# Kernel optimization log

Hardware: AMD Instinct MI355X
Metric: run time of the kernel (lower is better)

The kernel has to match this reference:

```python
import jax, jax.numpy as jnp
import numpy as np

D_MODEL = 1024
HEADS = 16
D_K = D_MODEL // HEADS
D_FF = 4096
EPS = 1e-6


def setup_inputs() -> dict:
    key = jax.random.key(0)
    ks = jax.random.split(key, 20)
    B, S, D = 8, 1024, D_MODEL
    sc = 1.0 / np.sqrt(D)
    scf = 1.0 / np.sqrt(D_FF)
    inp = {
        "x": jax.random.normal(ks[0], (B, S, D), jnp.float32),
        "mask": jnp.ones((B, 1, 1, S), jnp.int32),
        "wq": jax.random.normal(ks[1], (D, D), jnp.float32) * sc,
        "bq": jnp.zeros((D,), jnp.float32),
        "wk": jax.random.normal(ks[2], (D, D), jnp.float32) * sc,
        "bk": jnp.zeros((D,), jnp.float32),
        "wv": jax.random.normal(ks[3], (D, D), jnp.float32) * sc,
        "bv": jnp.zeros((D,), jnp.float32),
        "wo": jax.random.normal(ks[4], (D, D), jnp.float32) * sc,
        "bo": jnp.zeros((D,), jnp.float32),
        "w1": jax.random.normal(ks[5], (D_FF, D), jnp.float32) * sc,
        "b1": jnp.zeros((D_FF,), jnp.float32),
        "w2": jax.random.normal(ks[6], (D, D_FF), jnp.float32) * scf,
        "b2": jnp.zeros((D,), jnp.float32),
        "g1": jnp.ones((D,), jnp.float32),
        "be1": jnp.zeros((D,), jnp.float32),
        "g2": jnp.ones((D,), jnp.float32),
        "be2": jnp.zeros((D,), jnp.float32),
    }
    return inp


def _layernorm(x, gamma, beta):
    # Faithful to custom LayerNorm: unbiased std (ddof=1), divide by (std+eps)
    mean = jnp.mean(x, axis=-1, keepdims=True)
    std = jnp.std(x, axis=-1, ddof=1, keepdims=True)
    return gamma * (x - mean) / (std + EPS) + beta


def _mha(x, mask, wq, bq, wk, bk, wv, bv, wo, bo):
    B, S, D = x.shape
    q = x @ wq.T + bq
    k = x @ wk.T + bk
    v = x @ wv.T + bv
    # [B,S,D] -> [B,H,S,dk]
    q = q.reshape(B, S, HEADS, D_K).transpose(0, 2, 1, 3)
    k = k.reshape(B, S, HEADS, D_K).transpose(0, 2, 1, 3)
    v = v.reshape(B, S, HEADS, D_K).transpose(0, 2, 1, 3)
    scores = jnp.einsum("bhqd,bhkd->bhqk", q, k) / np.sqrt(D_K).astype(np.float32)
    scores = jnp.where(mask == 0, jnp.float32(-1e9), scores)
    attn = jax.nn.softmax(scores, axis=-1)
    out = jnp.einsum("bhqk,bhkd->bhqd", attn, v)
    out = out.transpose(0, 2, 1, 3).reshape(B, S, D)
    return out @ wo.T + bo


def reference(x, mask, wq, bq, wk, bk, wv, bv, wo, bo, w1, b1, w2, b2, g1, be1, g2, be2):
    # residual 1: x + MHA(LN(x))
    h = _layernorm(x, g1, be1)
    x = x + _mha(h, mask, wq, bq, wk, bk, wv, bv, wo, bo)
    # residual 2: x + FFN(LN(x))
    h = _layernorm(x, g2, be2)
    ff = jax.nn.relu(h @ w1.T + b1) @ w2.T + b2
    return x + ff
```

## Files before the change

### kernel.cpp

```cpp
#include <hip/hip_runtime.h>

typedef __attribute__((ext_vector_type(8))) short short8;
typedef __attribute__((ext_vector_type(4))) short short4_t;
typedef __attribute__((ext_vector_type(4))) float floatx4;
typedef __attribute__((ext_vector_type(16))) float floatx16;

#define NTOK 8192
#define S_ 1024
#define DM 1024

__device__ __forceinline__ unsigned short f2b(float f) {
    union { float f; unsigned u; } v; v.f = f;
    unsigned r = v.u + 0x7FFF + ((v.u >> 16) & 1);
    return (unsigned short)(r >> 16);
}

__device__ __forceinline__ float b2f(unsigned short u) {
    union { unsigned u; float f; } v; v.u = ((unsigned)u) << 16;
    return v.f;
}

__device__ __forceinline__ void gl_lds16(const void* g, void* l) {
    __builtin_amdgcn_global_load_lds((const __attribute__((address_space(1))) void*)g,
                                     (__attribute__((address_space(3))) void*)l, 16, 0, 0);
}

__global__ __launch_bounds__(256) void prep_kernel(const float* __restrict__ wq,
                                                   const float* __restrict__ wk,
                                                   const float* __restrict__ wv,
                                                   const float* __restrict__ wo,
                                                   const float* __restrict__ w1,
                                                   const float* __restrict__ w2,
                                                   const float* __restrict__ bq,
                                                   const float* __restrict__ bk,
                                                   const float* __restrict__ bv,
                                                   const int* __restrict__ mask,
                                                   const float* __restrict__ x,
                                                   const float* __restrict__ g1,
                                                   const float* __restrict__ be1,
                                                   unsigned short* __restrict__ wqkv_bf,
                                                   unsigned short* __restrict__ wo_bf,
                                                   unsigned short* __restrict__ w1_bf,
                                                   unsigned short* __restrict__ w2_bf,
                                                   float* __restrict__ bqkv,
                                                   float* __restrict__ mbias,
                                                   int* __restrict__ mflags,
                                                   unsigned short* __restrict__ h_bf) {
    const int bid = blockIdx.x;
    const int t = threadIdx.x;
    if (bid < 12288) {
        const int q = bid * 256 + t;
        const float* src;
        unsigned short* dst;
        int lq;
        if (q < 786432) {
            src = (q < 262144) ? wq : (q < 524288 ? wk : wv);
            lq = q & 262143;
            dst = wqkv_bf + (size_t)(q >> 18) * 1048576;
        } else if (q < 1048576) {
            src = wo; lq = q - 786432; dst = wo_bf;
        } else if (q < 2097152) {
            src = w1; lq = q - 1048576; dst = w1_bf;
        } else {
            src = w2; lq = q - 2097152; dst = w2_bf;
        }
        const float4 v = *reinterpret_cast<const float4*>(src + (size_t)lq * 4);
        short4_t o;
        o.x = (short)f2b(v.x); o.y = (short)f2b(v.y);
        o.z = (short)f2b(v.z); o.w = (short)f2b(v.w);
        *reinterpret_cast<short4_t*>(dst + (size_t)lq * 4) = o;
        return;
    }
    if (bid == 12288) {
#pragma unroll
        for (int it = 0; it < 3; ++it) {
            const int q = t + it * 256;
            const float* src = (q < 256) ? bq : (q < 512 ? bk : bv);
            const int lq = q & 255;
            *reinterpret_cast<float4*>(bqkv + q * 4) =
                *reinterpret_cast<const float4*>(src + lq * 4);
        }
        return;
    }
    if (bid == 12289) {
#pragma unroll
        for (int it = 0; it < 8; ++it) {
            const int q = t + it * 256;
            const int4 m = *reinterpret_cast<const int4*>(mask + q * 4);
            float4 o;
            o.x = (m.x == 0) ? -1e9f : 0.f;
            o.y = (m.y == 0) ? -1e9f : 0.f;
            o.z = (m.z == 0) ? -1e9f : 0.f;
            o.w = (m.w == 0) ? -1e9f : 0.f;
            *reinterpret_cast<float4*>(mbias + q * 4) = o;
        }
        if (t < 128) {
            int f = 0;
            const int* mp = mask + t * 64;
#pragma unroll
            for (int k = 0; k < 64; ++k) f |= (mp[k] == 0) ? 1 : 0;
            mflags[t] = f;
        }
        return;
    }
    const int row = bid - 12290;
    const float4 xv = *reinterpret_cast<const float4*>(x + (size_t)row * DM + t * 4);
    float s = xv.x + xv.y + xv.z + xv.w;
#pragma unroll
    for (int off = 32; off > 0; off >>= 1) s += __shfl_down(s, off);
    __shared__ float red[8];
    const int wid = t >> 6, lane = t & 63;
    if (lane == 0) red[wid] = s;
    __syncthreads();
    const float mean = (red[0] + red[1] + red[2] + red[3]) * (1.f / 1024.f);
    const float dx = xv.x - mean, dy = xv.y - mean, dz = xv.z - mean, dw = xv.w - mean;
    float ss = dx * dx + dy * dy + dz * dz + dw * dw;
#pragma unroll
    for (int off = 32; off > 0; off >>= 1) ss += __shfl_down(ss, off);
    if (lane == 0) red[4 + wid] = ss;
    __syncthreads();
    const float var = (red[4] + red[5] + red[6] + red[7]) * (1.f / 1023.f);
    const float inv = 1.f / (sqrtf(var) + 1e-6f);
    const float4 gv = *reinterpret_cast<const float4*>(g1 + t * 4);
    const float4 bev = *reinterpret_cast<const float4*>(be1 + t * 4);
    short4_t o;
    o.x = (short)f2b(gv.x * dx * inv + bev.x);
    o.y = (short)f2b(gv.y * dy * inv + bev.y);
    o.z = (short)f2b(gv.z * dz * inv + bev.z);
    o.w = (short)f2b(gv.w * dw * inv + bev.w);
    *reinterpret_cast<short4_t*>(h_bf + (size_t)row * DM + t * 4) = o;
}

__global__ __launch_bounds__(256) void ln_bf16(const unsigned short* __restrict__ xb,
                                               const float* __restrict__ g,
                                               const float* __restrict__ be,
                                               unsigned short* __restrict__ out) {
    const int row = blockIdx.x;
    const int t = threadIdx.x;
    const short4_t xv4 = *reinterpret_cast<const short4_t*>(xb + (size_t)row * DM + t * 4);
    float xv[4];
#pragma unroll
    for (int j = 0; j < 4; ++j) xv[j] = b2f((unsigned short)xv4[j]);
    float s = xv[0] + xv[1] + xv[2] + xv[3];
#pragma unroll
    for (int off = 32; off > 0; off >>= 1) s += __shfl_down(s, off);
    __shared__ float red[8];
    const int wid = t >> 6, lane = t & 63;
    if (lane == 0) red[wid] = s;
    __syncthreads();
    const float mean = (red[0] + red[1] + red[2] + red[3]) * (1.f / 1024.f);
    float d[4];
#pragma unroll
    for (int j = 0; j < 4; ++j) d[j] = xv[j] - mean;
    float ss = d[0] * d[0] + d[1] * d[1] + d[2] * d[2] + d[3] * d[3];
#pragma unroll
    for (int off = 32; off > 0; off >>= 1) ss += __shfl_down(ss, off);
    if (lane == 0) red[4 + wid] = ss;
    __syncthreads();
    const float var = (red[4] + red[5] + red[6] + red[7]) * (1.f / 1023.f);
    const float inv = 1.f / (sqrtf(var) + 1e-6f);
    const float4 gv = *reinterpret_cast<const float4*>(g + t * 4);
    const float4 bev = *reinterpret_cast<const float4*>(be + t * 4);
    short4_t o;
    o.x = (short)f2b(gv.x * d[0] * inv + bev.x);
    o.y = (short)f2b(gv.y * d[1] * inv + bev.y);
    o.z = (short)f2b(gv.z * d[2] * inv + bev.z);
    o.w = (short)f2b(gv.w * d[3] * inv + bev.w);
    *reinterpret_cast<short4_t*>(out + (size_t)row * DM + t * 4) = o;
}

template <int EPI>
__global__ __launch_bounds__(256, 2) void gemm_bt(const unsigned short* __restrict__ A,
                                                  const unsigned short* __restrict__ Bm,
                                                  const float* __restrict__ bias,
                                                  const void* __restrict__ res,
                                                  void* __restrict__ outp,
                                                  int M, int N, int K, int tilesX) {
    __shared__ __align__(16) unsigned short lds[2][2][8192];
    const int t = threadIdx.x;
    const int lane = t & 63, wid = t >> 6;
    const int wr = wid >> 1, wc = wid & 1;

    const int bid = blockIdx.x;
    const int xcd = bid & 7;
    const int lid = bid >> 3;
    const int sid = lid >> 5;
    const int off = lid & 31;
    const int gsid = sid * 8 + xcd;
    const int supercols = tilesX >> 2;
    const int srow = gsid / supercols;
    const int scol = gsid - srow * supercols;
    const int rowBase = (srow * 8 + (off >> 2)) * 128;
    const int colBase = (scol * 4 + (off & 3)) * 128;

    const int NT = K >> 6;
    const int lr31 = lane & 31;
    const int kh = lane >> 5;

    const unsigned short* Ag[4];
    const unsigned short* Bg[4];
#pragma unroll
    for (int j = 0; j < 4; ++j) {
        const int L = j * 256 + t;
        const int r = L >> 3;
        const int c = ((L & 7) ^ (r & 7)) * 8;
        Ag[j] = A + (size_t)(rowBase + r) * K + c;
        Bg[j] = Bm + (size_t)(colBase + r) * K + c;
    }

    floatx16 acc[2][2] = {};

#pragma unroll
    for (int j = 0; j < 4; ++j) gl_lds16(Ag[j], &lds[0][0][j * 2048 + wid * 512]);
#pragma unroll
    for (int j = 0; j < 4; ++j) gl_lds16(Bg[j], &lds[0][1][j * 2048 + wid * 512]);
#pragma unroll
    for (int j = 0; j < 4; ++j) { Ag[j] += 64; Bg[j] += 64; }

    int cur = 0;
    for (int tt = 0; tt < NT; ++tt) {
        if (tt + 1 < NT) {
#pragma unroll
            for (int j = 0; j < 4; ++j)
                gl_lds16(Ag[j], &lds[cur ^ 1][0][j * 2048 + wid * 512]);
#pragma unroll
            for (int j = 0; j < 4; ++j)
                gl_lds16(Bg[j], &lds[cur ^ 1][1][j * 2048 + wid * 512]);
#pragma unroll
            for (int j = 0; j < 4; ++j) { Ag[j] += 64; Bg[j] += 64; }
            asm volatile("s_waitcnt vmcnt(8)" ::: "memory");
        } else {
            asm volatile("s_waitcnt vmcnt(0)" ::: "memory");
        }
        __builtin_amdgcn_s_barrier();
        __builtin_amdgcn_sched_barrier(0);
        const unsigned short* Ab = &lds[cur][0][0];
        const unsigned short* Bb = &lds[cur][1][0];
#pragma unroll
        for (int ks = 0; ks < 4; ++ks) {
            short8 af[2], bfr[2];
#pragma unroll
            for (int mf = 0; mf < 2; ++mf) {
                const int r = wr * 64 + mf * 32 + lr31;
                const int cp = (ks * 2 + kh) ^ (r & 7);
                af[mf] = *reinterpret_cast<const short8*>(&Ab[r * 64 + cp * 8]);
            }
#pragma unroll
            for (int nf = 0; nf < 2; ++nf) {
                const int r = wc * 64 + nf * 32 + lr31;
                const int cp = (ks * 2 + kh) ^ (r & 7);
                bfr[nf] = *reinterpret_cast<const short8*>(&Bb[r * 64 + cp * 8]);
            }
            __builtin_amdgcn_s_setprio(1);
#pragma unroll
            for (int mf = 0; mf < 2; ++mf)
#pragma unroll
                for (int nf = 0; nf < 2; ++nf)
                    acc[mf][nf] = __builtin_amdgcn_mfma_f32_32x32x16_bf16(af[mf], bfr[nf], acc[mf][nf], 0, 0, 0);
            __builtin_amdgcn_s_setprio(0);
        }
        __builtin_amdgcn_sched_barrier(0);
        __builtin_amdgcn_s_barrier();
        cur ^= 1;
    }

    const int rbw = rowBase + wr * 64;
    const int cbw = colBase + wc * 64;
    const int lc31 = lane & 31;
    if (EPI == 4) {
        unsigned short* qh = (unsigned short*)outp;
        const float SC2 = 0.18033688f;
#pragma unroll
        for (int nf = 0; nf < 2; ++nf) {
            const int c = cbw + nf * 32 + lc31;
            const float bn = bias[c];
            const int sect = c >> 10;
            const int hh = (c >> 6) & 15;
            const int dd = c & 63;
            const float scl = (sect == 0) ? SC2 : 1.f;
#pragma unroll
            for (int mf = 0; mf < 2; ++mf) {
#pragma unroll
                for (int rg = 0; rg < 4; ++rg) {
                    const int r0 = rbw + mf * 32 + rg * 8 + 4 * kh;
                    const int bb = r0 >> 10, ss = r0 & 1023;
                    if (sect == 2) {
                        short4_t pk;
#pragma unroll
                        for (int j = 0; j < 4; ++j) pk[j] = (short)f2b(acc[mf][nf][rg * 4 + j] + bn);
                        *reinterpret_cast<short4_t*>(
                            &qh[16777216 + ((size_t)((bb * 16 + hh) * 64 + dd)) * 1024 + ss]) = pk;
                    } else {
                        unsigned short* base = qh + sect * 8388608;
#pragma unroll
                        for (int j = 0; j < 4; ++j)
                            base[((size_t)((bb * 16 + hh) * 1024 + ss + j)) * 64 + dd] =
                                f2b((acc[mf][nf][rg * 4 + j] + bn) * scl);
                    }
                }
            }
        }
        return;
    }
#pragma unroll
    for (int nf = 0; nf < 2; ++nf) {
        const int c = cbw + nf * 32 + lc31;
        const float bn = bias[c];
#pragma unroll
        for (int mf = 0; mf < 2; ++mf) {
#pragma unroll
            for (int rg = 0; rg < 4; ++rg) {
#pragma unroll
                for (int j = 0; j < 4; ++j) {
                    const int r = rbw + mf * 32 + rg * 8 + 4 * kh + j;
                    if (EPI == 2) {
                        const float v = acc[mf][nf][rg * 4 + j] + bn +
                                        ((const float*)res)[(size_t)r * N + c];
                        ((unsigned short*)outp)[(size_t)r * N + c] = f2b(v);
                    } else {
                        const float v = acc[mf][nf][rg * 4 + j] + bn +
                                        b2f(((const unsigned short*)res)[(size_t)r * N + c]);
                        ((float*)outp)[(size_t)r * N + c] = v;
                    }
                }
            }
        }
    }
}

__global__ __launch_bounds__(512, 2) void gemm256p(const unsigned short* __restrict__ A,
                                                   const unsigned short* __restrict__ Bm,
                                                   const float* __restrict__ bias,
                                                   unsigned short* __restrict__ outp,
                                                   int M, int N, int K, int tilesX) {
    __shared__ __align__(16) unsigned short Abuf[2][16384];
    __shared__ __align__(16) unsigned short Bbuf[2][16384];
    const int t = threadIdx.x;
    const int lane = t & 63, wid = t >> 6;
    const int wr = wid >> 2, wc = wid & 3;

    const int bid = blockIdx.x;
    const int xcd = bid & 7;
    const int lid = bid >> 3;
    const int sid = lid >> 5;
    const int off = lid & 31;
    const int gsid = sid * 8 + xcd;
    const int supercols = tilesX >> 2;
    const int srow = gsid / supercols;
    const int scol = gsid - srow * supercols;
    const int rowBase = (srow * 8 + (off >> 2)) * 256;
    const int colBase = (scol * 4 + (off & 3)) * 256;

    const int NT = K >> 6;
    const int lr31 = lane & 31;
    const int kh = lane >> 5;
    const int x7 = lane & 7;

    const int rho_s = t >> 3;
    const int csrc = ((t & 7) ^ (rho_s & 7)) * 8;
    const int ldst = t * 8;
    const unsigned short* Bs_[2][2];
    const unsigned short* As_[2][2];
#pragma unroll
    for (int h = 0; h < 2; ++h)
#pragma unroll
        for (int j = 0; j < 2; ++j) {
            const int rr = rho_s + j * 64;
            Bs_[h][j] = Bm + (size_t)(colBase + h * 128 + rr) * K + csrc;
            As_[h][j] = A + (size_t)(rowBase + ((rr >> 6) * 128 + h * 64 + (rr & 63))) * K + csrc;
        }

#define STG_BH(h_, b_, kk_)                                                   \
    do {                                                                      \
        gl_lds16(Bs_[h_][0] + (kk_), &Bbuf[b_][(h_)*8192 + ldst]);            \
        gl_lds16(Bs_[h_][1] + (kk_), &Bbuf[b_][(h_)*8192 + 4096 + ldst]);     \
    } while (0)
#define STG_AH(h_, b_, kk_)                                                   \
    do {                                                                      \
        gl_lds16(As_[h_][0] + (kk_), &Abuf[b_][(h_)*8192 + ldst]);            \
        gl_lds16(As_[h_][1] + (kk_), &Abuf[b_][(h_)*8192 + 4096 + ldst]);     \
    } while (0)

    floatx16 acc[4][2] = {};

    STG_BH(0, 0, 0); STG_BH(1, 0, 0); STG_AH(0, 0, 0); STG_AH(1, 0, 0);
    asm volatile("s_waitcnt vmcnt(0)" ::: "memory");
    __builtin_amdgcn_s_barrier();

    for (int kt = 0; kt < NT; ++kt) {
        const int cur = kt & 1, nxt = cur ^ 1;
        const bool pf = (kt + 1 < NT);
        const int kkn = (pf ? kt + 1 : kt) << 6;
        short8 bfr[2][4];
#pragma unroll
        for (int q = 0; q < 4; ++q) {
            short8 af[4];
            {
                const int rho = wr * 64 + (q & 1) * 32 + lr31;
                const unsigned short* Ab = &Abuf[cur][(q >> 1) * 8192];
#pragma unroll
                for (int s = 0; s < 4; ++s)
                    af[s] = *reinterpret_cast<const short8*>(
                        &Ab[rho * 64 + ((2 * s + kh) ^ x7) * 8]);
            }
            if (q == 0) {
#pragma unroll
                for (int nf = 0; nf < 2; ++nf) {
                    const int gcol = wc * 64 + nf * 32 + lr31;
                    const unsigned short* Bb = &Bbuf[cur][(gcol >> 7) * 8192];
                    const int rho = gcol & 127;
#pragma unroll
                    for (int s = 0; s < 4; ++s)
                        bfr[nf][s] = *reinterpret_cast<const short8*>(
                            &Bb[rho * 64 + ((2 * s + kh) ^ x7) * 8]);
                }
            }
            if (pf) {
                if (q == 0) STG_BH(0, nxt, kkn);
                if (q == 1) STG_BH(1, nxt, kkn);
                if (q == 2) STG_AH(0, nxt, kkn);
                if (q == 3) STG_AH(1, nxt, kkn);
            }
            __builtin_amdgcn_s_barrier();
            asm volatile("s_waitcnt lgkmcnt(0)" ::: "memory");
            __builtin_amdgcn_sched_barrier(0);
            __builtin_amdgcn_s_setprio(1);
#pragma unroll
            for (int s = 0; s < 4; ++s)
#pragma unroll
                for (int nf = 0; nf < 2; ++nf)
                    acc[q][nf] = __builtin_amdgcn_mfma_f32_32x32x16_bf16(af[s], bfr[nf][s], acc[q][nf], 0, 0, 0);
            __builtin_amdgcn_s_setprio(0);
            __builtin_amdgcn_sched_barrier(0);
            if (q == 1) {
                if (pf) asm volatile("s_waitcnt vmcnt(4)" ::: "memory");
                else    asm volatile("s_waitcnt vmcnt(0)" ::: "memory");
            }
            if (q == 3 && pf) asm volatile("s_waitcnt vmcnt(2)" ::: "memory");
            __builtin_amdgcn_s_barrier();
        }
    }
#undef STG_AH
#undef STG_BH

    const int rbw = rowBase + wr * 128;
    const int cbw = colBase + wc * 64;
    const int lc31 = lane & 31;
#pragma unroll
    for (int nf = 0; nf < 2; ++nf) {
        const int c = cbw + nf * 32 + lc31;
        const float bn = bias[c];
#pragma unroll
        for (int q = 0; q < 4; ++q) {
#pragma unroll
            for (int rg = 0; rg < 4; ++rg) {
                const int r0 = rbw + q * 32 + rg * 8 + 4 * kh;
#pragma unroll
                for (int j = 0; j < 4; ++j) {
                    const float v = fmaxf(acc[q][nf][rg * 4 + j] + bn, 0.f);
                    outp[(size_t)(r0 + j) * N + c] = f2b(v);
                }
            }
        }
    }
}

__global__ __launch_bounds__(256) void attn_mfma(const unsigned short* __restrict__ Qh,
                                                 const unsigned short* __restrict__ Kh,
                                                 const unsigned short* __restrict__ Vt,
                                                 const float* __restrict__ mbias,
                                                 const int* __restrict__ mflags,
                                                 unsigned short* __restrict__ out) {
    __shared__ __align__(16) unsigned short Kbuf[2][4096];
    __shared__ __align__(16) unsigned short Vbuf[2][4096];
    __shared__ __align__(16) unsigned short Pbuf[4][16][72];
    __shared__ __align__(16) float mk[1024];
    const int t = threadIdx.x;
    const int w = t >> 6, l = t & 63;
    const int g = l >> 4, q16 = l & 15;
    const int x7 = q16 & 7;
    const int bid = blockIdx.x;
    const int swz = (bid & 7) * 256 + (bid >> 3);
    const int bh = swz >> 4, qb = swz & 15;
    const int b = bh >> 4, h = bh & 15;

    const size_t qbase = ((size_t)bh * 1024 + qb * 64 + w * 16 + q16) * 64;
    const short8 qf0 = *reinterpret_cast<const short8*>(Qh + qbase + g * 8);
    const short8 qf1 = *reinterpret_cast<const short8*>(Qh + qbase + 32 + g * 8);

    const int r0 = t >> 3;
    const int c0 = ((t & 7) ^ (r0 & 7)) * 8;
    const unsigned short* Kg = Kh + (size_t)bh * 65536 + r0 * 64 + c0;
    const unsigned short* Vg = Vt + (size_t)bh * 65536 + r0 * 1024 + c0;

#define ATTN_STAGE(bi, kc_)                                                        \
    do {                                                                           \
        gl_lds16(Kg + (kc_) * 4096, &Kbuf[bi][w * 512]);                           \
        gl_lds16(Kg + (kc_) * 4096 + 2048, &Kbuf[bi][2048 + w * 512]);             \
        gl_lds16(Vg + (kc_) * 64, &Vbuf[bi][w * 512]);                             \
        gl_lds16(Vg + (kc_) * 64 + 32768, &Vbuf[bi][2048 + w * 512]);              \
    } while (0)

    gl_lds16(mbias + b * 1024 + t * 4, &mk[w * 256]);
    ATTN_STAGE(0, 0);

    floatx4 oacc[4] = {};
    floatx4 loacc = {};
    short8 ones;
#pragma unroll
    for (int j = 0; j < 8; ++j) ones[j] = (short)0x3F80;

    int cur = 0;
    for (int kc = 0; kc < 16; ++kc) {
        if (kc < 15) {
            ATTN_STAGE(cur ^ 1, kc + 1);
            asm volatile("s_waitcnt vmcnt(4)" ::: "memory");
        } else {
            asm volatile("s_waitcnt vmcnt(0)" ::: "memory");
        }
        __builtin_amdgcn_s_barrier();
        __builtin_amdgcn_sched_barrier(0);
        const unsigned short* Kb = Kbuf[cur];
        const unsigned short* Vb = Vbuf[cur];

        floatx4 st[4] = {};
        __builtin_amdgcn_s_setprio(1);
#pragma unroll
        for (int t4 = 0; t4 < 4; ++t4) {
            const int row = t4 * 16 + q16;
            const short8 kf0 = *reinterpret_cast<const short8*>(&Kb[row * 64 + (g ^ x7) * 8]);
            const short8 kf1 = *reinterpret_cast<const short8*>(&Kb[row * 64 + ((4 + g) ^ x7) * 8]);
            st[t4] = __builtin_amdgcn_mfma_f32_16x16x32_bf16(kf0, qf0, st[t4], 0, 0, 0);
            st[t4] = __builtin_amdgcn_mfma_f32_16x16x32_bf16(kf1, qf1, st[t4], 0, 0, 0);
        }
        __builtin_amdgcn_s_setprio(0);

        if (mflags[b * 16 + kc]) {
#pragma unroll
            for (int t4 = 0; t4 < 4; ++t4) {
                const float4 mbv = *reinterpret_cast<const float4*>(&mk[kc * 64 + t4 * 16 + g * 4]);
#pragma unroll
                for (int r = 0; r < 4; ++r) st[t4][r] += ((const float*)&mbv)[r];
            }
        }
#pragma unroll
        for (int t4 = 0; t4 < 4; ++t4) {
            const float p0 = __builtin_exp2f(st[t4][0]);
            const float p1 = __builtin_exp2f(st[t4][1]);
            const float p2 = __builtin_exp2f(st[t4][2]);
            const float p3 = __builtin_exp2f(st[t4][3]);
            unsigned u0, u1;
            asm("v_cvt_pk_bf16_f32 %0, %1, %2" : "=v"(u0) : "v"(p0), "v"(p1));
            asm("v_cvt_pk_bf16_f32 %0, %1, %2" : "=v"(u1) : "v"(p2), "v"(p3));
            uint2 pr; pr.x = u0; pr.y = u1;
            *reinterpret_cast<uint2*>(&Pbuf[w][q16][t4 * 16 + g * 4]) = pr;
        }

        const short8 pf0 = *reinterpret_cast<const short8*>(&Pbuf[w][q16][g * 8]);
        const short8 pf1 = *reinterpret_cast<const short8*>(&Pbuf[w][q16][32 + g * 8]);
        __builtin_amdgcn_s_setprio(1);
        loacc = __builtin_amdgcn_mfma_f32_16x16x32_bf16(pf0, ones, loacc, 0, 0, 0);
        loacc = __builtin_amdgcn_mfma_f32_16x16x32_bf16(pf1, ones, loacc, 0, 0, 0);
#pragma unroll
        for (int n = 0; n < 4; ++n) {
            const int row = n * 16 + q16;
            const short8 vf0 = *reinterpret_cast<const short8*>(&Vb[row * 64 + (g ^ x7) * 8]);
            const short8 vf1 = *reinterpret_cast<const short8*>(&Vb[row * 64 + ((4 + g) ^ x7) * 8]);
            oacc[n] = __builtin_amdgcn_mfma_f32_16x16x32_bf16(pf0, vf0, oacc[n], 0, 0, 0);
            oacc[n] = __builtin_amdgcn_mfma_f32_16x16x32_bf16(pf1, vf1, oacc[n], 0, 0, 0);
        }
        __builtin_amdgcn_s_setprio(0);
        __builtin_amdgcn_sched_barrier(0);
        __builtin_amdgcn_s_barrier();
        cur ^= 1;
    }
#undef ATTN_STAGE

    const size_t obase = ((size_t)b * S_ + qb * 64 + w * 16) * 1024 + h * 64;
#pragma unroll
    for (int r = 0; r < 4; ++r) {
        const float invr = 1.f / loacc[r];
        const size_t orow = obase + (size_t)(g * 4 + r) * 1024;
#pragma unroll
        for (int n = 0; n < 4; ++n)
            out[orow + n * 16 + q16] = f2b(oacc[n][r] * invr);
    }
}

extern "C" void kernel_launch(void* const* d_in, const int* in_sizes, int n_in,
                              void* d_out, int out_size, void* d_ws, size_t ws_size,
                              hipStream_t stream) {
    const float* x   = (const float*)d_in[0];
    const int*  mask = (const int*)d_in[1];
    const float* wq  = (const float*)d_in[2];
    const float* bq  = (const float*)d_in[3];
    const float* wk  = (const float*)d_in[4];
    const float* bk  = (const float*)d_in[5];
    const float* wv  = (const float*)d_in[6];
    const float* bv  = (const float*)d_in[7];
    const float* wo  = (const float*)d_in[8];
    const float* bo  = (const float*)d_in[9];
    const float* w1  = (const float*)d_in[10];
    const float* b1  = (const float*)d_in[11];
    const float* w2  = (const float*)d_in[12];
    const float* b2  = (const float*)d_in[13];
    const float* g1  = (const float*)d_in[14];
    const float* be1 = (const float*)d_in[15];
    const float* g2  = (const float*)d_in[16];
    const float* be2 = (const float*)d_in[17];

    char* ws = (char*)d_ws;
    unsigned short* wqkv_bf = (unsigned short*)(ws);
    unsigned short* wo_bf   = (unsigned short*)(ws + 6291456);
    unsigned short* w1_bf   = (unsigned short*)(ws + 8388608);
    unsigned short* w2_bf   = (unsigned short*)(ws + 16777216);
    float*          bqkv    = (float*)(ws + 25165824);
    float*          mbias   = (float*)(ws + 25178112);
    int*            mflags  = (int*)(ws + 25210880);
    unsigned short* h_bf    = (unsigned short*)(ws + 25214976);
    unsigned short* x1b     = (unsigned short*)(ws + 41992192);
    unsigned short* attn_bf = (unsigned short*)(ws + 75546624);
    unsigned short* qkvh    = (unsigned short*)(ws + 92323840);
    unsigned short* ff1_bf  = (unsigned short*)(ws + 92323840);

    prep_kernel<<<20482, 256, 0, stream>>>(wq, wk, wv, wo, w1, w2, bq, bk, bv, mask,
                                           x, g1, be1,
                                           wqkv_bf, wo_bf, w1_bf, w2_bf, bqkv, mbias, mflags, h_bf);

    gemm_bt<4><<<24 * 64, 256, 0, stream>>>(h_bf, wqkv_bf, bqkv, nullptr, qkvh, NTOK, 3072, 1024, 24);
    attn_mfma<<<2048, 256, 0, stream>>>(qkvh, qkvh + 8388608, qkvh + 16777216, mbias, mflags, attn_bf);
    gemm_bt<2><<<8 * 64, 256, 0, stream>>>(attn_bf, wo_bf, bo, x, x1b, NTOK, 1024, 1024, 8);
    ln_bf16<<<NTOK, 256, 0, stream>>>(x1b, g2, be2, h_bf);
    gemm256p<<<512, 512, 0, stream>>>(h_bf, w1_bf, b1, ff1_bf, NTOK, 4096, 1024, 16);
    gemm_bt<5><<<8 * 64, 256, 0, stream>>>(ff1_bf, w2_bf, b2, x1b, (float*)d_out, NTOK, 1024, 4096, 8);
}
```

Before: 356.2 us.

## Restructure FFN1 GEMM into two-k-tile unrolled pipeline with finer-grained prefetch staging

Replaces the 256x256 FFN1 GEMM's one-tile-per-iteration double buffer with a loop that processes two k-tiles per iteration. Each half-buffer (A or B) is refilled as soon as its last reader finishes, and the vmcnt waits are tuned so global-to-LDS loads overlap more of the MFMA work. Launch bounds drop to one block per CU. The goal is to hide memory latency better, at the cost of more complex wait-count bookkeeping, lower occupancy, and a reliance on an even number of k-tiles.

```diff
diff --git a/kernel.cpp b/kernel.cpp
--- a/kernel.cpp
+++ b/kernel.cpp
@@ -328,13 +328,13 @@
     }
 }
 
-__global__ __launch_bounds__(512, 2) void gemm256p(const unsigned short* __restrict__ A,
-                                                   const unsigned short* __restrict__ Bm,
-                                                   const float* __restrict__ bias,
-                                                   unsigned short* __restrict__ outp,
-                                                   int M, int N, int K, int tilesX) {
-    __shared__ __align__(16) unsigned short Abuf[2][16384];
-    __shared__ __align__(16) unsigned short Bbuf[2][16384];
+__global__ __launch_bounds__(512, 1) void gemm8p2(const unsigned short* __restrict__ A,
+                                                  const unsigned short* __restrict__ Bm,
+                                                  const float* __restrict__ bias,
+                                                  unsigned short* __restrict__ outp,
+                                                  int M, int N, int K, int tilesX) {
+    __shared__ __align__(16) unsigned short Abuf[2][2][8192];
+    __shared__ __align__(16) unsigned short Bbuf[2][2][8192];
     const int t = threadIdx.x;
     const int lane = t & 63, wid = t >> 6;
     const int wr = wid >> 2, wc = wid & 3;
@@ -352,6 +352,7 @@
     const int colBase = (scol * 4 + (off & 3)) * 256;
 
     const int NT = K >> 6;
+    const int NI = NT >> 1;
     const int lr31 = lane & 31;
     const int kh = lane >> 5;
     const int x7 = lane & 7;
@@ -370,78 +371,112 @@
             As_[h][j] = A + (size_t)(rowBase + ((rr >> 6) * 128 + h * 64 + (rr & 63))) * K + csrc;
         }
 
-#define STG_BH(h_, b_, kk_)                                                   \
+#define STG_B(h_, b_, kk_)                                                    \
     do {                                                                      \
-        gl_lds16(Bs_[h_][0] + (kk_), &Bbuf[b_][(h_)*8192 + ldst]);            \
-        gl_lds16(Bs_[h_][1] + (kk_), &Bbuf[b_][(h_)*8192 + 4096 + ldst]);     \
+        gl_lds16(Bs_[h_][0] + (kk_), &Bbuf[b_][h_][ldst]);                    \
+        gl_lds16(Bs_[h_][1] + (kk_), &Bbuf[b_][h_][4096 + ldst]);             \
     } while (0)
-#define STG_AH(h_, b_, kk_)                                                   \
+#define STG_A(h_, b_, kk_)                                                    \
     do {                                                                      \
-        gl_lds16(As_[h_][0] + (kk_), &Abuf[b_][(h_)*8192 + ldst]);            \
-        gl_lds16(As_[h_][1] + (kk_), &Abuf[b_][(h_)*8192 + 4096 + ldst]);     \
+        gl_lds16(As_[h_][0] + (kk_), &Abuf[b_][h_][ldst]);                    \
+        gl_lds16(As_[h_][1] + (kk_), &Abuf[b_][h_][4096 + ldst]);             \
     } while (0)
+#define RD_A(b_, q_, af_)                                                          \
+    do {                                                                           \
+        const unsigned short* Ab_ = &Abuf[b_][(q_) >> 1][0];                       \
+        const int rho_ = wr * 64 + ((q_) & 1) * 32 + lr31;                         \
+        _Pragma("unroll") for (int s = 0; s < 4; ++s)                              \
+            (af_)[s] = *reinterpret_cast<const short8*>(                           \
+                &Ab_[rho_ * 64 + ((2 * s + kh) ^ x7) * 8]);                        \
+    } while (0)
+#define RD_B(b_, bf_)                                                              \
+    do {                                                                           \
+        _Pragma("unroll") for (int nf = 0; nf < 2; ++nf) {                         \
+            const int gcol_ = wc * 64 + nf * 32 + lr31;                            \
+            const unsigned short* Bb_ = &Bbuf[b_][gcol_ >> 7][0];                  \
+            const int rho_ = gcol_ & 127;                                          \
+            _Pragma("unroll") for (int s = 0; s < 4; ++s)                          \
+                (bf_)[nf][s] = *reinterpret_cast<const short8*>(                   \
+                    &Bb_[rho_ * 64 + ((2 * s + kh) ^ x7) * 8]);                    \
+        }                                                                          \
+    } while (0)
+#define MFMA8(q_, af_, bf_)                                                        \
+    do {                                                                           \
+        __builtin_amdgcn_s_barrier();                                              \
+        asm volatile("s_waitcnt lgkmcnt(0)" ::: "memory");                         \
+        __builtin_amdgcn_sched_barrier(0);                                         \
+        __builtin_amdgcn_s_setprio(1);                                             \
+        _Pragma("unroll") for (int s = 0; s < 4; ++s)                              \
+            _Pragma("unroll") for (int nf = 0; nf < 2; ++nf)                       \
+                acc[q_][nf] = __builtin_amdgcn_mfma_f32_32x32x16_bf16(             \
+                    (af_)[s], (bf_)[nf][s], acc[q_][nf], 0, 0, 0);                 \
+        __builtin_amdgcn_s_setprio(0);                                             \
+        __builtin_amdgcn_sched_barrier(0);                                         \
+    } while (0)
 
     floatx16 acc[4][2] = {};
 
-    STG_BH(0, 0, 0); STG_BH(1, 0, 0); STG_AH(0, 0, 0); STG_AH(1, 0, 0);
+    STG_B(0, 0, 0); STG_B(1, 0, 0); STG_A(0, 0, 0); STG_A(1, 0, 0);
+    STG_B(0, 1, 64); STG_B(1, 1, 64); STG_A(0, 1, 64); STG_A(1, 1, 64);
     asm volatile("s_waitcnt vmcnt(0)" ::: "memory");
     __builtin_amdgcn_s_barrier();
 
-    for (int kt = 0; kt < NT; ++kt) {
-        const int cur = kt & 1, nxt = cur ^ 1;
-        const bool pf = (kt + 1 < NT);
-        const int kkn = (pf ? kt + 1 : kt) << 6;
+    for (int it = 0; it < NI; ++it) {
+        const int kk2 = (2 * it + 2) << 6;
+        const int kk1 = (2 * it + 1) << 6;
+        const bool pf = (2 * it + 2 < NT);
+        const bool last = (it == NI - 1);
+        short8 af[4];
         short8 bfr[2][4];
-#pragma unroll
-        for (int q = 0; q < 4; ++q) {
-            short8 af[4];
-            {
-                const int rho = wr * 64 + (q & 1) * 32 + lr31;
-                const unsigned short* Ab = &Abuf[cur][(q >> 1) * 8192];
-#pragma unroll
-                for (int s = 0; s < 4; ++s)
-                    af[s] = *reinterpret_cast<const short8*>(
-                        &Ab[rho * 64 + ((2 * s + kh) ^ x7) * 8]);
-            }
-            if (q == 0) {
-#pragma unroll
-                for (int nf = 0; nf < 2; ++nf) {
-                    const int gcol = wc * 64 + nf * 32 + lr31;
-                    const unsigned short* Bb = &Bbuf[cur][(gcol >> 7) * 8192];
-                    const int rho = gcol & 127;
-#pragma unroll
-                    for (int s = 0; s < 4; ++s)
-                        bfr[nf][s] = *reinterpret_cast<const short8*>(
-                            &Bb[rho * 64 + ((2 * s + kh) ^ x7) * 8]);
-                }
-            }
-            if (pf) {
-                if (q == 0) STG_BH(0, nxt, kkn);
-                if (q == 1) STG_BH(1, nxt, kkn);
-                if (q == 2) STG_AH(0, nxt, kkn);
-                if (q == 3) STG_AH(1, nxt, kkn);
-            }
-            __builtin_amdgcn_s_barrier();
-            asm volatile("s_waitcnt lgkmcnt(0)" ::: "memory");
-            __builtin_amdgcn_sched_barrier(0);
-            __builtin_amdgcn_s_setprio(1);
-#pragma unroll
-            for (int s = 0; s < 4; ++s)
-#pragma unroll
-                for (int nf = 0; nf < 2; ++nf)
-                    acc[q][nf] = __builtin_amdgcn_mfma_f32_32x32x16_bf16(af[s], bfr[nf][s], acc[q][nf], 0, 0, 0);
-            __builtin_amdgcn_s_setprio(0);
-            __builtin_amdgcn_sched_barrier(0);
-            if (q == 1) {
-                if (pf) asm volatile("s_waitcnt vmcnt(4)" ::: "memory");
-                else    asm volatile("s_waitcnt vmcnt(0)" ::: "memory");
-            }
-            if (q == 3 && pf) asm volatile("s_waitcnt vmcnt(2)" ::: "memory");
-            __builtin_amdgcn_s_barrier();
-        }
-    }
-#undef STG_AH
-#undef STG_BH
+
+        RD_A(0, 0, af);
+        RD_B(0, bfr);
+        if (it > 0) STG_A(1, 1, kk1);
+        MFMA8(0, af, bfr);
+        __builtin_amdgcn_s_barrier();
+        RD_A(0, 1, af);
+        if (pf) STG_B(0, 0, kk2);
+        MFMA8(1, af, bfr);
+        if (last) asm volatile("s_waitcnt vmcnt(2)" ::: "memory");
+        else      asm volatile("s_waitcnt vmcnt(10)" ::: "memory");
+        __builtin_amdgcn_s_barrier();
+        RD_A(0, 2, af);
+        if (pf) STG_B(1, 0, kk2);
+        MFMA8(2, af, bfr);
+        __builtin_amdgcn_s_barrier();
+        RD_A(0, 3, af);
+        if (pf) STG_A(0, 0, kk2);
+        MFMA8(3, af, bfr);
+        if (last) asm volatile("s_waitcnt vmcnt(2)" ::: "memory");
+        else      asm volatile("s_waitcnt vmcnt(8)" ::: "memory");
+        __builtin_amdgcn_s_barrier();
+        RD_A(1, 0, af);
+        RD_B(1, bfr);
+        if (pf) STG_A(1, 0, kk2);
+        MFMA8(0, af, bfr);
+        __builtin_amdgcn_s_barrier();
+        RD_A(1, 1, af);
+        if (pf) STG_B(0, 1, kk2 + 64);
+        MFMA8(1, af, bfr);
+        if (last) asm volatile("s_waitcnt vmcnt(0)" ::: "memory");
+        else      asm volatile("s_waitcnt vmcnt(10)" ::: "memory");
+        __builtin_amdgcn_s_barrier();
+        RD_A(1, 2, af);
+        if (pf) STG_B(1, 1, kk2 + 64);
+        MFMA8(2, af, bfr);
+        __builtin_amdgcn_s_barrier();
+        RD_A(1, 3, af);
+        if (pf) STG_A(0, 1, kk2 + 64);
+        MFMA8(3, af, bfr);
+        if (last) asm volatile("s_waitcnt vmcnt(0)" ::: "memory");
+        else      asm volatile("s_waitcnt vmcnt(8)" ::: "memory");
+        __builtin_amdgcn_s_barrier();
+    }
+#undef STG_A
+#undef STG_B
+#undef RD_A
+#undef RD_B
+#undef MFMA8
 
     const int rbw = rowBase + wr * 128;
     const int cbw = colBase + wc * 64;
@@ -631,6 +666,6 @@
     attn_mfma<<<2048, 256, 0, stream>>>(qkvh, qkvh + 8388608, qkvh + 16777216, mbias, mflags, attn_bf);
     gemm_bt<2><<<8 * 64, 256, 0, stream>>>(attn_bf, wo_bf, bo, x, x1b, NTOK, 1024, 1024, 8);
     ln_bf16<<<NTOK, 256, 0, stream>>>(x1b, g2, be2, h_bf);
-    gemm256p<<<512, 512, 0, stream>>>(h_bf, w1_bf, b1, ff1_bf, NTOK, 4096, 1024, 16);
+    gemm8p2<<<512, 512, 0, stream>>>(h_bf, w1_bf, b1, ff1_bf, NTOK, 4096, 1024, 16);
     gemm_bt<5><<<8 * 64, 256, 0, stream>>>(ff1_bf, w2_bf, b2, x1b, (float*)d_out, NTOK, 1024, 4096, 8);
 }
```

New measurement: 357.6 us. Within noise of the previous version (+0.4%).
